# Kernel tuning notes

Hardware: AMD Instinct MI355X
Metric: run time of the kernel (lower is better)

## Reference

```python
import jax, jax.numpy as jnp
import numpy as np
from jax.scipy.special import logsumexp

HEADS = 8
BUCKETS = 64
DIM = 64
TEMPERATURE = 0.7
SINKHORN_ITER = 8
EPS = 1e-06


def setup_inputs() -> dict:
    key = jax.random.key(0)
    k1, k2, k3, k4, k5 = jax.random.split(key, 5)
    bh, seq = 32, 8192
    q = jax.random.normal(k1, (bh, seq, DIM), dtype=jnp.float32)
    k = jax.random.normal(k2, (bh, seq, DIM), dtype=jnp.float32)
    q_pos_emb = jax.random.normal(k3, (1, HEADS, BUCKETS, DIM), dtype=jnp.float32)
    k_pos_emb = jax.random.normal(k4, (1, HEADS, BUCKETS, DIM), dtype=jnp.float32)
    # gumbel noise: -log(-log(u)) with the module's eps, same shape as R
    u = jax.random.uniform(k5, (bh, BUCKETS, BUCKETS), dtype=jnp.float32)
    gumbel = -jnp.log(-jnp.log(u + EPS) + EPS)
    return {"q": q, "k": k, "q_pos_emb": q_pos_emb, "k_pos_emb": k_pos_emb, "gumbel": gumbel}


def _expand_merge(pos, b):
    # (1, heads, buckets, dim) -> (b*heads, buckets, dim)
    _, h, bu, d = pos.shape
    return jnp.broadcast_to(pos, (b, h, bu, d)).reshape(b * h, bu, d)


def reference(q, k, q_pos_emb, k_pos_emb, gumbel):
    bh, seq, d = q.shape
    b = bh // HEADS
    # bucket + mean over bucket contents: (bh, buckets, seq//buckets, d) -> (bh, buckets, d)
    b_q = q.reshape(bh, BUCKETS, -1, d).mean(axis=2)
    b_k = k.reshape(bh, BUCKETS, -1, d).mean(axis=2)
    sq = b_q + _expand_merge(q_pos_emb, b)
    sk = b_k + _expand_merge(k_pos_emb, b)
    R = jnp.einsum('bie,bje->bij', sq, sk)  # (bh, buckets, buckets)
    # gumbel_sinkhorn(relu(R))
    r = jnp.log(jax.nn.relu(R) + EPS)
    r = (r + gumbel) / TEMPERATURE

    def step(r, _):
        r = r - logsumexp(r, axis=2, keepdims=True)
        r = r - logsumexp(r, axis=1, keepdims=True)
        return r, None

    r, _ = jax.lax.scan(step, r, None, length=SINKHORN_ITER)
    return jnp.exp(r)
```

## Files before the change

kernel.cpp:

```cpp
#include <hip/hip_runtime.h>
#include <math.h>

#define HEADS 8
#define BUCKETS 64
#define DIM 64
#define SEQ 8192
#define BH 32
#define ROWS_PER_BUCKET (SEQ / BUCKETS)
#define EPS 1e-6f
#define LOG2E 1.4426950408889634f
#define INV_T (1.0f / 0.7f)
#define SINKHORN_ITER_COUNT 8

typedef float f4 __attribute__((ext_vector_type(4)));

static __device__ __forceinline__ float fast_exp2(float x) {
#if __has_builtin(__builtin_amdgcn_exp2f)
    return __builtin_amdgcn_exp2f(x);
#else
    return exp2f(x);
#endif
}
static __device__ __forceinline__ float fast_log2(float x) {
#if __has_builtin(__builtin_amdgcn_logf)
    return __builtin_amdgcn_logf(x);
#else
    return log2f(x);
#endif
}

__global__ __launch_bounds__(256) void bucket_mean_kernel(
    const float* __restrict__ q, const float* __restrict__ k,
    const float* __restrict__ q_pos, const float* __restrict__ k_pos,
    float* __restrict__ sq, float* __restrict__ sk) {

    const int lane = threadIdx.x & 63;
    const int task = blockIdx.x * 4 + (threadIdx.x >> 6);
    const int which = task >> 11;
    const int bh = (task >> 6) & 31;
    const int bucket = task & 63;

    const float* __restrict__ src = which ? k : q;
    const float* __restrict__ pos = which ? k_pos : q_pos;
    float* __restrict__ dst = which ? sk : sq;

    const int c = lane & 15;
    const int rs = lane >> 4;

    const f4* __restrict__ s4 = (const f4*)(src
        + ((size_t)bh * SEQ + (size_t)bucket * ROWS_PER_BUCKET) * DIM);

    const int head = bh & (HEADS - 1);
    f4 p = ((const f4*)pos)[(head * BUCKETS + bucket) * (DIM / 4) + c];

    f4 acc = (f4)(0.f);
#pragma unroll
    for (int i = 0; i < 32; ++i) {
        f4 v = __builtin_nontemporal_load(&s4[(size_t)(i * 4 + rs) * (DIM / 4) + c]);
        acc += v;
    }

#pragma unroll
    for (int off = 16; off <= 32; off <<= 1) {
        acc[0] += __shfl_xor(acc[0], off);
        acc[1] += __shfl_xor(acc[1], off);
        acc[2] += __shfl_xor(acc[2], off);
        acc[3] += __shfl_xor(acc[3], off);
    }

    const float inv = 1.0f / (float)ROWS_PER_BUCKET;
    f4 r = acc * inv + p;

    if (lane < 16)
        ((f4*)dst)[(bh * BUCKETS + bucket) * (DIM / 4) + c] = r;
}

__global__ __launch_bounds__(1024) void sinkhorn_kernel(
    const float* __restrict__ sq, const float* __restrict__ sk,
    const float* __restrict__ gumbel, float* __restrict__ out) {

    const int bh = blockIdx.x;
    const int t = threadIdx.x;
    const int lane = t & 63;
    const int w = t >> 6;

    __shared__ float sq_s[64][64];
    __shared__ float sk_s[64][65];
    __shared__ float r_s[64][65];

    {
        const float4* __restrict__ sq4 = (const float4*)(sq + bh * 4096);
        const float4* __restrict__ sk4 = (const float4*)(sk + bh * 4096);
        int row = t >> 4, ch = t & 15;
        float4 v = sq4[t];
        *(float4*)&sq_s[row][ch * 4] = v;
        float4 u = sk4[t];
        sk_s[row][ch * 4 + 0] = u.x; sk_s[row][ch * 4 + 1] = u.y;
        sk_s[row][ch * 4 + 2] = u.z; sk_s[row][ch * 4 + 3] = u.w;
    }
    __syncthreads();

    float acc[4];
#pragma unroll
    for (int ii = 0; ii < 4; ++ii) acc[ii] = 0.f;
    for (int d = 0; d < 64; ++d) {
        float skv = sk_s[lane][d];
#pragma unroll
        for (int ii = 0; ii < 4; ++ii)
            acc[ii] = fmaf(sq_s[w * 4 + ii][d], skv, acc[ii]);
    }

    const float* __restrict__ g = gumbel + bh * 4096;
#pragma unroll
    for (int ii = 0; ii < 4; ++ii) {
        int i = w * 4 + ii;
        float Rp = fmaxf(acc[ii], 0.f) + EPS;
        float y = (fast_log2(Rp) + g[i * 64 + lane] * LOG2E) * INV_T;
        r_s[i][lane] = y;
    }
    __syncthreads();

    for (int it = 0; it < SINKHORN_ITER_COUNT; ++it) {
#pragma unroll
        for (int ii = 0; ii < 4; ++ii) {
            int i = w * 4 + ii;
            float x = r_s[i][lane];
            float s = fast_exp2(x);
#pragma unroll
            for (int off = 32; off > 0; off >>= 1) s += __shfl_xor(s, off);
            r_s[i][lane] = x - fast_log2(s);
        }
        __syncthreads();
#pragma unroll
        for (int jj = 0; jj < 4; ++jj) {
            int jc = w * 4 + jj;
            float x = r_s[lane][jc];
            float s = fast_exp2(x);
#pragma unroll
            for (int off = 32; off > 0; off >>= 1) s += __shfl_xor(s, off);
            r_s[lane][jc] = x - fast_log2(s);
        }
        __syncthreads();
    }

    float* __restrict__ o = out + bh * 4096;
#pragma unroll
    for (int ii = 0; ii < 4; ++ii) {
        int i = w * 4 + ii;
        o[i * 64 + lane] = fast_exp2(r_s[i][lane]);
    }
}

extern "C" void kernel_launch(void* const* d_in, const int* in_sizes, int n_in,
                              void* d_out, int out_size, void* d_ws, size_t ws_size,
                              hipStream_t stream) {
    const float* q   = (const float*)d_in[0];
    const float* k   = (const float*)d_in[1];
    const float* qpe = (const float*)d_in[2];
    const float* kpe = (const float*)d_in[3];
    const float* gum = (const float*)d_in[4];
    float* out = (float*)d_out;

    float* sq = (float*)d_ws;
    float* sk = sq + BH * BUCKETS * DIM;

    bucket_mean_kernel<<<1024, 256, 0, stream>>>(q, k, qpe, kpe, sq, sk);
    sinkhorn_kernel<<<BH, 1024, 0, stream>>>(sq, sk, gum, out);
}
```

Baseline: 49.87 us.

## Stream bucket rows through LDS with double-buffered direct global-to-LDS loads

Replaces the per-lane nontemporal register loads in the bucket-mean kernel with global_load_lds transfers into a per-wave double-buffered LDS region, consumed in four batches under explicit vmcnt/lgkmcnt waits. The aim is to keep more bytes in flight per wave and overlap the accumulation with outstanding loads, which matters because this kernel is bandwidth-bound on 64 MB of input. In exchange it uses 64 KB of LDS per block, which may limit occupancy, and it depends on hand-placed waitcnt and scheduling barriers being correct.

```diff
diff --git a/kernel.cpp b/kernel.cpp
--- a/kernel.cpp
+++ b/kernel.cpp
@@ -13,6 +13,8 @@
 #define SINKHORN_ITER_COUNT 8
 
 typedef float f4 __attribute__((ext_vector_type(4)));
+#define AS3 __attribute__((address_space(3)))
+#define AS1 __attribute__((address_space(1)))
 
 static __device__ __forceinline__ float fast_exp2(float x) {
 #if __has_builtin(__builtin_amdgcn_exp2f)
@@ -34,8 +36,11 @@
     const float* __restrict__ q_pos, const float* __restrict__ k_pos,
     float* __restrict__ sq, float* __restrict__ sk) {
 
+    __shared__ float lds[4 * 2 * 2048];
+
     const int lane = threadIdx.x & 63;
-    const int task = blockIdx.x * 4 + (threadIdx.x >> 6);
+    const int wid = threadIdx.x >> 6;
+    const int task = blockIdx.x * 4 + wid;
     const int which = task >> 11;
     const int bh = (task >> 6) & 31;
     const int bucket = task & 63;
@@ -44,21 +49,59 @@
     const float* __restrict__ pos = which ? k_pos : q_pos;
     float* __restrict__ dst = which ? sk : sq;
 
+    const float* src_blk = src + ((size_t)bh * SEQ + (size_t)bucket * ROWS_PER_BUCKET) * DIM;
+    float* wlds = &lds[wid * 4096];
+
     const int c = lane & 15;
     const int rs = lane >> 4;
 
-    const f4* __restrict__ s4 = (const f4*)(src
-        + ((size_t)bh * SEQ + (size_t)bucket * ROWS_PER_BUCKET) * DIM);
-
     const int head = bh & (HEADS - 1);
     f4 p = ((const f4*)pos)[(head * BUCKETS + bucket) * (DIM / 4) + c];
 
+    auto issue = [&](int buf, int batch) {
+        const float* g0 = src_blk + batch * 2048 + lane * 4;
+#pragma unroll
+        for (int inst = 0; inst < 8; ++inst) {
+            __builtin_amdgcn_global_load_lds(
+                (const AS1 void*)(g0 + inst * 256),
+                (AS3 void*)((AS3 float*)&wlds[buf * 2048 + inst * 256]),
+                16, 0, 0);
+        }
+    };
+
     f4 acc = (f4)(0.f);
-#pragma unroll
-    for (int i = 0; i < 32; ++i) {
-        f4 v = __builtin_nontemporal_load(&s4[(size_t)(i * 4 + rs) * (DIM / 4) + c]);
-        acc += v;
-    }
+    auto consume = [&](int buf) {
+#pragma unroll
+        for (int i = 0; i < 8; ++i) {
+            f4 v = *(const f4*)&wlds[buf * 2048 + (4 * i + rs) * 64 + c * 4];
+            acc += v;
+        }
+    };
+
+    issue(0, 0);
+    issue(1, 1);
+
+    asm volatile("s_waitcnt vmcnt(8)" ::: "memory");
+    __builtin_amdgcn_sched_barrier(0);
+    consume(0);
+    asm volatile("s_waitcnt lgkmcnt(0)" ::: "memory");
+    __builtin_amdgcn_sched_barrier(0);
+    issue(0, 2);
+
+    asm volatile("s_waitcnt vmcnt(8)" ::: "memory");
+    __builtin_amdgcn_sched_barrier(0);
+    consume(1);
+    asm volatile("s_waitcnt lgkmcnt(0)" ::: "memory");
+    __builtin_amdgcn_sched_barrier(0);
+    issue(1, 3);
+
+    asm volatile("s_waitcnt vmcnt(8)" ::: "memory");
+    __builtin_amdgcn_sched_barrier(0);
+    consume(0);
+
+    asm volatile("s_waitcnt vmcnt(0)" ::: "memory");
+    __builtin_amdgcn_sched_barrier(0);
+    consume(1);
 
 #pragma unroll
     for (int off = 16; off <= 32; off <<= 1) {
```

After: 50.16 us. About the same (+0.6%).
